# Kernel tuning notes

Measured on AMD Instinct MI355X. Metric: run time of the kernel, lower is better.

Reference implementation:

```python
import jax, jax.numpy as jnp
import numpy as np

H = 1024
B, S = 8, 2048
EPS = 1e-5


def _layernorm(x, w, b):
    m = jnp.mean(x, axis=-1, keepdims=True)
    v = jnp.mean((x - m) ** 2, axis=-1, keepdims=True)
    return (x - m) * jax.lax.rsqrt(v + EPS) * w + b


def setup_inputs() -> dict:
    key = jax.random.key(0)
    ks = jax.random.split(key, 10)
    x = jax.random.normal(ks[0], (B, S, H), dtype=jnp.float32)
    # LayerNorm params (torch default init: weight=1, bias=0)
    qn_w = jnp.ones((H,), jnp.float32)
    qn_b = jnp.zeros((H,), jnp.float32)
    kvn_w = jnp.ones((H,), jnp.float32)
    kvn_b = jnp.zeros((H,), jnp.float32)
    # q_prime/k_prime/v_prime ~ U(-0.5, 0.5)
    q_prime = jax.random.uniform(ks[1], (1, H), jnp.float32) - 0.5
    k_prime = jax.random.uniform(ks[2], (1, H), jnp.float32) - 0.5
    v_prime = jax.random.uniform(ks[3], (1, H), jnp.float32) - 0.5
    # Linear params, torch-style fan_in init
    lim = 1.0 / np.sqrt(H)
    qW = jax.random.uniform(ks[4], (H, H), jnp.float32, -lim, lim)
    qb = jax.random.uniform(ks[5], (H,), jnp.float32, -lim, lim)
    v1W = jax.random.uniform(ks[6], (H, H), jnp.float32, -lim, lim)
    v1b = jax.random.uniform(ks[7], (H,), jnp.float32, -lim, lim)
    v2W = jax.random.uniform(ks[8], (H, H), jnp.float32, -lim, lim)
    v2b = jax.random.uniform(ks[9], (H,), jnp.float32, -lim, lim)
    return {"x": x, "qn_w": qn_w, "qn_b": qn_b, "kvn_w": kvn_w, "kvn_b": kvn_b,
            "q_prime": q_prime, "k_prime": k_prime, "v_prime": v_prime,
            "qW": qW, "qb": qb, "v1W": v1W, "v1b": v1b, "v2W": v2W, "v2b": v2b}


def reference(x, qn_w, qn_b, kvn_w, kvn_b, q_prime, k_prime, v_prime,
              qW, qb, v1W, v1b, v2W, v2b):
    divisor = jnp.sqrt(jnp.float32(x.shape[-1]))
    xqn = _layernorm(x, qn_w, qn_b)            # [B,S,H]
    xkvn = _layernorm(x, kvn_w, kvn_b)         # [B,S,H]
    kr = xkvn * jax.nn.sigmoid(k_prime)        # [B,S,H]
    qr = (xqn @ qW.T + qb) * jax.nn.sigmoid(q_prime)  # [B,S,H]
    vp = jax.nn.sigmoid(v_prime)               # [1,H]
    gate = jax.nn.sigmoid(vp @ v1W.T + v1b) * jnp.tanh(vp @ v2W.T + v2b)  # [1,H]
    vr = xkvn * gate                           # [B,S,H]
    scores = jnp.einsum('bsh,bth->bst', qr, kr) / divisor  # [B,S,S]
    b, s, t = scores.shape
    # global softmax over flattened seq x seq matrix
    attn = jax.nn.softmax(scores.reshape(b, s * t), axis=-1).reshape(b, s, t)
    attended = jnp.einsum('bst,bth->bsh', attn, vr)
    return attended + xqn
```

## Files before the change

### kernel.cpp

```cpp
#include <hip/hip_runtime.h>
#include <stdint.h>


#define DEVI __device__ __forceinline__

typedef __bf16 bf16x8 __attribute__((ext_vector_type(8)));
typedef float  f32x4  __attribute__((ext_vector_type(4)));

typedef __attribute__((address_space(3))) uint32_t lds_u32_t;
typedef __attribute__((address_space(1))) uint32_t glb_u32_t;

DEVI uint16_t f2bf(float f) {
  union { float f; uint32_t u; } v; v.f = f;
  uint32_t r = (v.u + 0x7fffu + ((v.u >> 16) & 1u)) >> 16;
  return (uint16_t)r;
}
DEVI float bf2f(uint16_t b) {
  union { uint32_t u; float f; } v; v.u = ((uint32_t)b) << 16;
  return v.f;
}
DEVI float sigm(float x) { return 1.0f / (1.0f + __expf(-x)); }

DEVI void gl_lds16(const void* g, const void* lds_base) {
  __builtin_amdgcn_global_load_lds((glb_u32_t*)(uintptr_t)g,
                                   (lds_u32_t*)(uint32_t)(uintptr_t)lds_base,
                                   16, 0, 0);
}


#define SLOT (256 * 32)

DEVI void stage_half(const uint16_t* __restrict__ src, size_t ld, int kbase,
                     uint16_t* slot, int tid) {
#pragma unroll
  for (int q = 0; q < 2; q++) {
    const int idx = q * 512 + tid;
    const int r = idx >> 2;
    const int cl = (((idx & 3) ^ ((r >> 1) & 3)) * 8);
    gl_lds16(src + (size_t)r * ld + (kbase + cl),
             slot + (size_t)(q * 512 + (tid & ~63)) * 8);
  }
}

DEVI void gemm256(const uint16_t* __restrict__ A, size_t lda,
                  const uint16_t* __restrict__ B, size_t ldb,
                  int K, uint16_t* sA, uint16_t* sB, f32x4 (&acc)[8][4])
{
  const int tid = threadIdx.x, lane = tid & 63, w = tid >> 6;
  const int wr = (w >> 2) * 128, wc = (w & 3) * 64;
  const int m16 = lane & 15, quad = lane >> 4;
  const int NT = K >> 6, NH = K >> 5;

  stage_half(A, lda, 0, sA, tid);
  stage_half(B, ldb, 0, sB, tid);
  stage_half(A, lda, 32, sA + SLOT, tid);
  stage_half(B, ldb, 32, sB + SLOT, tid);
  stage_half(A, lda, 64, sA + 2 * SLOT, tid);
  stage_half(B, ldb, 64, sB + 2 * SLOT, tid);
  asm volatile("s_waitcnt vmcnt(4)" ::: "memory");
  __builtin_amdgcn_s_barrier();

  const int sw = (quad ^ ((m16 >> 1) & 3)) * 8;

  for (int t = 0; t < NT; t++) {
#pragma unroll
    for (int p = 0; p < 4; p++) {
      const int ks = p >> 1, g = p & 1;
      const uint16_t* a_s = sA + ((2 * t + ks) & 3) * SLOT;
      const uint16_t* b_s = sB + ((2 * t + ks) & 3) * SLOT;
      bf16x8 af[4], bv[4];
#pragma unroll
      for (int i = 0; i < 4; i++) {
        af[i] = *(const bf16x8*)(a_s + (wr + g * 64 + i * 16 + m16) * 32 + sw);
        bv[i] = *(const bf16x8*)(b_s + (wc + i * 16 + m16) * 32 + sw);
      }
      const int h = 2 * t + 3 + ks;
      if (h < NH) {
        if (g == 0) stage_half(A, lda, h * 32, sA + (h & 3) * SLOT, tid);
        else        stage_half(B, ldb, h * 32, sB + (h & 3) * SLOT, tid);
      }
      __builtin_amdgcn_s_barrier();
      __builtin_amdgcn_s_setprio(1);
#pragma unroll
      for (int mi = 0; mi < 4; mi++)
#pragma unroll
        for (int ni = 0; ni < 4; ni++)
          acc[g * 4 + mi][ni] = __builtin_amdgcn_mfma_f32_16x16x32_bf16(
              af[mi], bv[ni], acc[g * 4 + mi][ni], 0, 0, 0);
      __builtin_amdgcn_s_setprio(0);
      if (p == 3) {
        if (t < NT - 2) asm volatile("s_waitcnt vmcnt(4)" ::: "memory");
        else            asm volatile("s_waitcnt vmcnt(0)" ::: "memory");
      }
      __builtin_amdgcn_s_barrier();
    }
  }
}

__global__ void gate_kernel(const float* __restrict__ v_prime,
                            const float* __restrict__ v1W, const float* __restrict__ v1b,
                            const float* __restrict__ v2W, const float* __restrict__ v2b,
                            const float* __restrict__ k_prime,
                            float* __restrict__ gate2)
{
  const int tid = threadIdx.x, lane = tid & 63, w = tid >> 6;
  const int j = blockIdx.x * 4 + w;
  float d1 = 0.f, d2 = 0.f;
  for (int it = 0; it < 16; it++) {
    int i = it * 64 + lane;
    float vp = sigm(v_prime[i]);
    d1 += vp * v1W[(size_t)j * 1024 + i];
    d2 += vp * v2W[(size_t)j * 1024 + i];
  }
  for (int off = 32; off; off >>= 1) { d1 += __shfl_xor(d1, off); d2 += __shfl_xor(d2, off); }
  if (lane == 0)
    gate2[j] = sigm(d1 + v1b[j]) * tanhf(d2 + v2b[j]) / sigm(k_prime[j]);
}

__global__ void cvt_kernel(const float* __restrict__ src, uint16_t* __restrict__ dst)
{
  size_t i = ((size_t)blockIdx.x * 256 + threadIdx.x) * 4;
  float4 v = *(const float4*)(src + i);
  *(ushort4*)(dst + i) = make_ushort4(f2bf(v.x), f2bf(v.y), f2bf(v.z), f2bf(v.w));
}

__global__ __launch_bounds__(256) void ln_kernel(
    const float* __restrict__ x,
    const float* __restrict__ qn_w, const float* __restrict__ qn_b,
    const float* __restrict__ kvn_w, const float* __restrict__ kvn_b,
    const float* __restrict__ k_prime,
    uint16_t* __restrict__ xqn_bf, uint16_t* __restrict__ kr,
    float* __restrict__ krowsq)
{
  const int lane = threadIdx.x & 63, w = threadIdx.x >> 6;
  const int row = blockIdx.x * 4 + w;
  const float4* xr = (const float4*)(x + (size_t)row * 1024);
  float4 v[4];
  float s = 0.f, sq = 0.f;
#pragma unroll
  for (int i = 0; i < 4; i++) {
    v[i] = xr[i * 64 + lane];
    s  += v[i].x + v[i].y + v[i].z + v[i].w;
    sq += v[i].x * v[i].x + v[i].y * v[i].y + v[i].z * v[i].z + v[i].w * v[i].w;
  }
  for (int off = 32; off; off >>= 1) { s += __shfl_xor(s, off); sq += __shfl_xor(sq, off); }
  const float mean = s * (1.f / 1024.f);
  const float rstd = rsqrtf(sq * (1.f / 1024.f) - mean * mean + 1e-5f);

  float ksq = 0.f;
  const size_t o4 = (size_t)row * 256;
#pragma unroll
  for (int i = 0; i < 4; i++) {
    const int idx = i * 64 + lane;
    float4 qw = ((const float4*)qn_w)[idx],  qb4 = ((const float4*)qn_b)[idx];
    float4 kw = ((const float4*)kvn_w)[idx], kb4 = ((const float4*)kvn_b)[idx];
    float4 kp = ((const float4*)k_prime)[idx];
    float xn0 = (v[i].x - mean) * rstd, xn1 = (v[i].y - mean) * rstd;
    float xn2 = (v[i].z - mean) * rstd, xn3 = (v[i].w - mean) * rstd;
    float xq0 = xn0 * qw.x + qb4.x, xq1 = xn1 * qw.y + qb4.y;
    float xq2 = xn2 * qw.z + qb4.z, xq3 = xn3 * qw.w + qb4.w;
    float xk0 = xn0 * kw.x + kb4.x, xk1 = xn1 * kw.y + kb4.y;
    float xk2 = xn2 * kw.z + kb4.z, xk3 = xn3 * kw.w + kb4.w;
    float k0 = xk0 * sigm(kp.x), k1 = xk1 * sigm(kp.y);
    float k2 = xk2 * sigm(kp.z), k3 = xk3 * sigm(kp.w);
    ksq += k0 * k0 + k1 * k1 + k2 * k2 + k3 * k3;
    ((ushort4*)xqn_bf)[o4 + idx] = make_ushort4(f2bf(xq0), f2bf(xq1), f2bf(xq2), f2bf(xq3));
    ((ushort4*)kr)[o4 + idx] = make_ushort4(f2bf(k0), f2bf(k1), f2bf(k2), f2bf(k3));
  }
  for (int off = 32; off; off >>= 1) ksq += __shfl_xor(ksq, off);
  if (lane == 0) krowsq[row] = ksq;
}

__global__ __launch_bounds__(512, 2) void qr_gemm_kernel(
    const uint16_t* __restrict__ xqn_bf, const uint16_t* __restrict__ qWbf,
    const float* __restrict__ qb, const float* __restrict__ q_prime,
    uint16_t* __restrict__ qr, float* __restrict__ qnormsq)
{
  __shared__ uint16_t sA[4 * SLOT], sB[4 * SLOT];
  const int lid = blockIdx.x;
  const int c = lid >> 6, r = lid & 63;
  f32x4 acc[8][4];
#pragma unroll
  for (int i = 0; i < 8; i++)
#pragma unroll
    for (int j = 0; j < 4; j++) acc[i][j] = (f32x4)0.0f;

  gemm256(xqn_bf + (size_t)r * 256 * 1024, 1024,
          qWbf + (size_t)c * 256 * 1024, 1024, 1024, sA, sB, acc);

  const int tid = threadIdx.x, lane = tid & 63, w = tid >> 6;
  const int m16 = lane & 15, quad = lane >> 4;
  const int rbase = r * 256 + (w >> 2) * 128, cbase = c * 256 + (w & 3) * 64;
#pragma unroll
  for (int ai = 0; ai < 8; ai++) {
    const int gr0 = rbase + (ai >> 2) * 64 + (ai & 3) * 16 + quad * 4;
    float rsq[4] = {0.f, 0.f, 0.f, 0.f};
#pragma unroll
    for (int ni = 0; ni < 4; ni++) {
      const int gc = cbase + ni * 16 + m16;
      const float scale = sigm(q_prime[gc]);
      const float bias = qb[gc];
#pragma unroll
      for (int rr = 0; rr < 4; rr++) {
        float val = (acc[ai][ni][rr] + bias) * scale;
        qr[(size_t)(gr0 + rr) * 1024 + gc] = f2bf(val);
        rsq[rr] += val * val;
      }
    }
#pragma unroll
    for (int rr = 0; rr < 4; rr++) {
      float tq = rsq[rr];
      tq += __shfl_xor(tq, 1); tq += __shfl_xor(tq, 2);
      tq += __shfl_xor(tq, 4); tq += __shfl_xor(tq, 8);
      if (m16 == 0) atomicAdd(&qnormsq[gr0 + rr], tq);
    }
  }
}

__global__ void bound_kernel(const float* __restrict__ qnormsq,
                             const float* __restrict__ krowsq, float* __restrict__ MZ)
{
  const int b = blockIdx.x, tid = threadIdx.x, lane = tid & 63, w = tid >> 6;
  float mq = 0.f, mk = 0.f;
  for (int i = tid; i < 2048; i += 256) {
    mq = fmaxf(mq, qnormsq[b * 2048 + i]);
    mk = fmaxf(mk, krowsq[b * 2048 + i]);
  }
  for (int off = 32; off; off >>= 1) {
    mq = fmaxf(mq, __shfl_xor(mq, off));
    mk = fmaxf(mk, __shfl_xor(mk, off));
  }
  __shared__ float rm[4], rk[4];
  if (lane == 0) { rm[w] = mq; rk[w] = mk; }
  __syncthreads();
  if (tid == 0) {
    float qmax = fmaxf(fmaxf(rm[0], rm[1]), fmaxf(rm[2], rm[3]));
    float kmax = fmaxf(fmaxf(rk[0], rk[1]), fmaxf(rk[2], rk[3]));
    MZ[b] = sqrtf(qmax * kmax) * 0.03125f;
  }
}

__global__ void transpose_kernel(const uint16_t* __restrict__ kr,
                                 const float* __restrict__ gate2,
                                 uint16_t* __restrict__ vrt)
{
  __shared__ uint16_t t[64 * 72];
  const int b = blockIdx.z;
  const int t0 = blockIdx.x * 64, h0 = blockIdx.y * 64;
  const uint16_t* src = kr + (size_t)b * 2048 * 1024;
#pragma unroll
  for (int p = 0; p < 2; p++) {
    int flat = p * 256 + threadIdx.x;
    int r = flat >> 3, c = (flat & 7) * 8;
    *(uint4*)(&t[r * 72 + c]) = *(const uint4*)(src + (size_t)(t0 + r) * 1024 + h0 + c);
  }
  __syncthreads();
  uint16_t* dst = vrt + (size_t)b * 1024 * 2048;
#pragma unroll
  for (int p = 0; p < 2; p++) {
    int flat = p * 256 + threadIdx.x;
    int oh = flat >> 3, oc = (flat & 7) * 8;
    const float g = gate2[h0 + oh];
    union { uint16_t e[8]; uint4 v; } u;
#pragma unroll
    for (int j = 0; j < 8; j++) u.e[j] = f2bf(bf2f(t[(oc + j) * 72 + oh]) * g);
    *(uint4*)(dst + (size_t)(h0 + oh) * 2048 + t0 + oc) = u.v;
  }
}

__global__ __launch_bounds__(512, 2) void scores_kernel(
    const uint16_t* __restrict__ qr, const uint16_t* __restrict__ kr,
    const float* __restrict__ MZ,
    uint16_t* __restrict__ scores, float* __restrict__ blockZ)
{
  __shared__ uint16_t sA[4 * SLOT], sB[4 * SLOT];
  __shared__ float redz[8];
  const int lid = blockIdx.x;
  const int b = lid >> 6, c = (lid >> 3) & 7, r = lid & 7;
  f32x4 acc[8][4];
#pragma unroll
  for (int i = 0; i < 8; i++)
#pragma unroll
    for (int j = 0; j < 4; j++) acc[i][j] = (f32x4)0.0f;

  gemm256(qr + (size_t)b * 2048 * 1024 + (size_t)r * 256 * 1024, 1024,
          kr + (size_t)b * 2048 * 1024 + (size_t)c * 256 * 1024, 1024,
          1024, sA, sB, acc);

  const float Mhat = MZ[b];
  const int tid = threadIdx.x, lane = tid & 63, w = tid >> 6;
  const int m16 = lane & 15, quad = lane >> 4;
  const int rbase = r * 256 + (w >> 2) * 128, cbase = c * 256 + (w & 3) * 64;
  uint16_t* S = scores + ((size_t)b << 22);
  float zt = 0.f;
#pragma unroll
  for (int ai = 0; ai < 8; ai++) {
    const int gr0 = rbase + (ai >> 2) * 64 + (ai & 3) * 16 + quad * 4;
#pragma unroll
    for (int ni = 0; ni < 4; ni++) {
      const int gc = cbase + ni * 16 + m16;
#pragma unroll
      for (int rr = 0; rr < 4; rr++) {
        float pe = __expf(acc[ai][ni][rr] * 0.03125f - Mhat);
        zt += pe;
        S[(size_t)(gr0 + rr) * 2048 + gc] = f2bf(pe);
      }
    }
  }
  for (int off = 32; off; off >>= 1) zt += __shfl_xor(zt, off);
  if (lane == 0) redz[w] = zt;
  __syncthreads();
  if (tid == 0) {
    float sz = 0.f;
#pragma unroll
    for (int i = 0; i < 8; i++) sz += redz[i];
    blockZ[lid] = sz;
  }
}

__global__ void zreduce_kernel(const float* __restrict__ blockZ, float* __restrict__ MZ)
{
  const int b = blockIdx.x, lane = threadIdx.x;
  float z = blockZ[b * 64 + lane];
  for (int off = 32; off; off >>= 1) z += __shfl_xor(z, off);
  if (lane == 0) MZ[8 + b] = z;
}

__global__ __launch_bounds__(512, 2) void pv_gemm_kernel(
    const uint16_t* __restrict__ P, const uint16_t* __restrict__ vrt,
    const float* __restrict__ MZ, const uint16_t* __restrict__ xqn_bf,
    float* __restrict__ out)
{
  __shared__ uint16_t sA[4 * SLOT], sB[4 * SLOT];
  const int lid = blockIdx.x;
  const int b = lid >> 5, c = (lid >> 3) & 3, r = lid & 7;
  f32x4 acc[8][4];
#pragma unroll
  for (int i = 0; i < 8; i++)
#pragma unroll
    for (int j = 0; j < 4; j++) acc[i][j] = (f32x4)0.0f;

  gemm256(P + ((size_t)b << 22) + (size_t)r * 256 * 2048, 2048,
          vrt + (size_t)b * 1024 * 2048 + (size_t)c * 256 * 2048, 2048,
          2048, sA, sB, acc);

  const float invZ = 1.0f / MZ[8 + b];
  const int tid = threadIdx.x, lane = tid & 63, w = tid >> 6;
  const int m16 = lane & 15, quad = lane >> 4;
  const int rbase = r * 256 + (w >> 2) * 128, cbase = c * 256 + (w & 3) * 64;
#pragma unroll
  for (int ai = 0; ai < 8; ai++) {
    const int gr0 = rbase + (ai >> 2) * 64 + (ai & 3) * 16 + quad * 4;
#pragma unroll
    for (int ni = 0; ni < 4; ni++) {
      const int gc = cbase + ni * 16 + m16;
#pragma unroll
      for (int rr = 0; rr < 4; rr++) {
        size_t o = ((size_t)b * 2048 + gr0 + rr) * 1024 + gc;
        out[o] = acc[ai][ni][rr] * invZ + bf2f(xqn_bf[o]);
      }
    }
  }
}

extern "C" void kernel_launch(void* const* d_in, const int* in_sizes, int n_in,
                              void* d_out, int out_size, void* d_ws, size_t ws_size,
                              hipStream_t stream) {
  const float* x       = (const float*)d_in[0];
  const float* qn_w    = (const float*)d_in[1];
  const float* qn_b    = (const float*)d_in[2];
  const float* kvn_w   = (const float*)d_in[3];
  const float* kvn_b   = (const float*)d_in[4];
  const float* q_prime = (const float*)d_in[5];
  const float* k_prime = (const float*)d_in[6];
  const float* v_prime = (const float*)d_in[7];
  const float* qW      = (const float*)d_in[8];
  const float* qb      = (const float*)d_in[9];
  const float* v1W     = (const float*)d_in[10];
  const float* v1b     = (const float*)d_in[11];
  const float* v2W     = (const float*)d_in[12];
  const float* v2b     = (const float*)d_in[13];
  float* out = (float*)d_out;

  const size_t BS = 16384, H = 1024;
  char* ws = (char*)d_ws;
  size_t off = 0;
  auto alloc = [&](size_t bytes) -> char* {
    char* p = ws + off;
    off = (off + bytes + 255) & ~(size_t)255;
    return p;
  };
  float*    gate2   = (float*)alloc(H * 4);
  float*    MZ      = (float*)alloc(16 * 4);
  float*    blockZ  = (float*)alloc(2048 * 4);
  float*    qnormsq = (float*)alloc(16384 * 4);
  float*    krowsq  = (float*)alloc(16384 * 4);
  uint16_t* qWbf    = (uint16_t*)alloc(H * H * 2);
  uint16_t* xqn_bf  = (uint16_t*)alloc(BS * H * 2);
  uint16_t* kr      = (uint16_t*)alloc(BS * H * 2);
  uint16_t* scores  = (uint16_t*)alloc(BS * H * 2 * 2);
  uint16_t* vrt     = (uint16_t*)alloc(BS * H * 2);
  uint16_t* qr      = (uint16_t*)alloc(BS * H * 2);

  hipMemsetAsync(qnormsq, 0, 16384 * 4, stream);
  gate_kernel<<<256, 256, 0, stream>>>(v_prime, v1W, v1b, v2W, v2b, k_prime, gate2);
  cvt_kernel<<<1024, 256, 0, stream>>>(qW, qWbf);
  ln_kernel<<<4096, 256, 0, stream>>>(x, qn_w, qn_b, kvn_w, kvn_b, k_prime,
                                      xqn_bf, kr, krowsq);
  qr_gemm_kernel<<<256, 512, 0, stream>>>(xqn_bf, qWbf, qb, q_prime, qr, qnormsq);
  transpose_kernel<<<dim3(32, 16, 8), 256, 0, stream>>>(kr, gate2, vrt);
  bound_kernel<<<8, 256, 0, stream>>>(qnormsq, krowsq, MZ);
  scores_kernel<<<512, 512, 0, stream>>>(qr, kr, MZ, scores, blockZ);
  zreduce_kernel<<<8, 64, 0, stream>>>(blockZ, MZ);
  pv_gemm_kernel<<<256, 512, 0, stream>>>(scores, vrt, MZ, xqn_bf, out);
}
```

Baseline: 381.2 us.

## Software-pipeline LDS fragment loads one phase ahead of MFMA clusters in gemm256

Restructures the GEMM inner loop so that LDS fragment reads for the next MFMA cluster are issued before the current cluster executes, reusing B fragments across two A half-tiles instead of reloading them. Global-to-LDS staging is reordered to interleave B and A halves, and each phase uses one barrier instead of two. The aim is to hide LDS read latency behind MFMA work and cut redundant ds_reads and barriers. In exchange it raises register pressure from holding six fragment arrays, and it relies on subtle barrier and vmcnt ordering for correctness of the 4-slot ring buffer.

```diff
diff --git a/kernel.cpp b/kernel.cpp
--- a/kernel.cpp
+++ b/kernel.cpp
@@ -42,6 +42,16 @@
   }
 }
 
+#define MFMA_CLUSTER(AF, BV, GOFF)                                          \
+  __builtin_amdgcn_s_setprio(1);                                            \
+  _Pragma("unroll")                                                         \
+  for (int mi = 0; mi < 4; mi++)                                            \
+    _Pragma("unroll")                                                       \
+    for (int ni = 0; ni < 4; ni++)                                          \
+      acc[(GOFF) + mi][ni] = __builtin_amdgcn_mfma_f32_16x16x32_bf16(       \
+          AF[mi], BV[ni], acc[(GOFF) + mi][ni], 0, 0, 0);                   \
+  __builtin_amdgcn_s_setprio(0);
+
 DEVI void gemm256(const uint16_t* __restrict__ A, size_t lda,
                   const uint16_t* __restrict__ B, size_t ldb,
                   int K, uint16_t* sA, uint16_t* sB, f32x4 (&acc)[8][4])
@@ -50,50 +60,72 @@
   const int wr = (w >> 2) * 128, wc = (w & 3) * 64;
   const int m16 = lane & 15, quad = lane >> 4;
   const int NT = K >> 6, NH = K >> 5;
-
+  const int sw = (quad ^ ((m16 >> 1) & 3)) * 8;
+
+  stage_half(B, ldb, 0, sB, tid);
   stage_half(A, lda, 0, sA, tid);
-  stage_half(B, ldb, 0, sB, tid);
+  stage_half(B, ldb, 32, sB + SLOT, tid);
   stage_half(A, lda, 32, sA + SLOT, tid);
-  stage_half(B, ldb, 32, sB + SLOT, tid);
+  stage_half(B, ldb, 64, sB + 2 * SLOT, tid);
   stage_half(A, lda, 64, sA + 2 * SLOT, tid);
-  stage_half(B, ldb, 64, sB + 2 * SLOT, tid);
   asm volatile("s_waitcnt vmcnt(4)" ::: "memory");
   __builtin_amdgcn_s_barrier();
 
-  const int sw = (quad ^ ((m16 >> 1) & 3)) * 8;
+  bf16x8 bv_a[4], af_a[4], af_b[4], bv_c[4], af_c[4], af_d[4];
+#pragma unroll
+  for (int i = 0; i < 4; i++) {
+    bv_a[i] = *(const bf16x8*)(sB + (wc + i * 16 + m16) * 32 + sw);
+    af_a[i] = *(const bf16x8*)(sA + (wr + i * 16 + m16) * 32 + sw);
+  }
 
   for (int t = 0; t < NT; t++) {
-#pragma unroll
-    for (int p = 0; p < 4; p++) {
-      const int ks = p >> 1, g = p & 1;
-      const uint16_t* a_s = sA + ((2 * t + ks) & 3) * SLOT;
-      const uint16_t* b_s = sB + ((2 * t + ks) & 3) * SLOT;
-      bf16x8 af[4], bv[4];
+    const uint16_t* a0 = sA + ((2 * t) & 3) * SLOT;
+    const uint16_t* a1 = sA + ((2 * t + 1) & 3) * SLOT;
+    const uint16_t* b1 = sB + ((2 * t + 1) & 3) * SLOT;
+
+#pragma unroll
+    for (int i = 0; i < 4; i++)
+      af_b[i] = *(const bf16x8*)(a0 + (wr + 64 + i * 16 + m16) * 32 + sw);
+    if (2 * t + 3 < NH)
+      stage_half(B, ldb, (2 * t + 3) * 32, sB + ((2 * t + 3) & 3) * SLOT, tid);
+    __builtin_amdgcn_s_barrier();
+    MFMA_CLUSTER(af_a, bv_a, 0)
+
+#pragma unroll
+    for (int i = 0; i < 4; i++) {
+      bv_c[i] = *(const bf16x8*)(b1 + (wc + i * 16 + m16) * 32 + sw);
+      af_c[i] = *(const bf16x8*)(a1 + (wr + i * 16 + m16) * 32 + sw);
+    }
+    if (2 * t + 3 < NH)
+      stage_half(A, lda, (2 * t + 3) * 32, sA + ((2 * t + 3) & 3) * SLOT, tid);
+    if (t < NT - 2) asm volatile("s_waitcnt vmcnt(4)" ::: "memory");
+    else            asm volatile("s_waitcnt vmcnt(0)" ::: "memory");
+    __builtin_amdgcn_s_barrier();
+    MFMA_CLUSTER(af_b, bv_a, 4)
+
+#pragma unroll
+    for (int i = 0; i < 4; i++)
+      af_d[i] = *(const bf16x8*)(a1 + (wr + 64 + i * 16 + m16) * 32 + sw);
+    if (2 * t + 4 < NH)
+      stage_half(B, ldb, (2 * t + 4) * 32, sB + ((2 * t + 4) & 3) * SLOT, tid);
+    __builtin_amdgcn_s_barrier();
+    MFMA_CLUSTER(af_c, bv_c, 0)
+
+    if (t + 1 < NT) {
+      const uint16_t* a2 = sA + ((2 * t + 2) & 3) * SLOT;
+      const uint16_t* b2 = sB + ((2 * t + 2) & 3) * SLOT;
 #pragma unroll
       for (int i = 0; i < 4; i++) {
-        af[i] = *(const bf16x8*)(a_s + (wr + g * 64 + i * 16 + m16) * 32 + sw);
-        bv[i] = *(const bf16x8*)(b_s + (wc + i * 16 + m16) * 32 + sw);
+        bv_a[i] = *(const bf16x8*)(b2 + (wc + i * 16 + m16) * 32 + sw);
+        af_a[i] = *(const bf16x8*)(a2 + (wr + i * 16 + m16) * 32 + sw);
       }
-      const int h = 2 * t + 3 + ks;
-      if (h < NH) {
-        if (g == 0) stage_half(A, lda, h * 32, sA + (h & 3) * SLOT, tid);
-        else        stage_half(B, ldb, h * 32, sB + (h & 3) * SLOT, tid);
-      }
-      __builtin_amdgcn_s_barrier();
-      __builtin_amdgcn_s_setprio(1);
-#pragma unroll
-      for (int mi = 0; mi < 4; mi++)
-#pragma unroll
-        for (int ni = 0; ni < 4; ni++)
-          acc[g * 4 + mi][ni] = __builtin_amdgcn_mfma_f32_16x16x32_bf16(
-              af[mi], bv[ni], acc[g * 4 + mi][ni], 0, 0, 0);
-      __builtin_amdgcn_s_setprio(0);
-      if (p == 3) {
-        if (t < NT - 2) asm volatile("s_waitcnt vmcnt(4)" ::: "memory");
-        else            asm volatile("s_waitcnt vmcnt(0)" ::: "memory");
-      }
-      __builtin_amdgcn_s_barrier();
-    }
+    }
+    if (2 * t + 4 < NH)
+      stage_half(A, lda, (2 * t + 4) * 32, sA + ((2 * t + 4) & 3) * SLOT, tid);
+    if (t < NT - 2) asm volatile("s_waitcnt vmcnt(4)" ::: "memory");
+    else            asm volatile("s_waitcnt vmcnt(0)" ::: "memory");
+    __builtin_amdgcn_s_barrier();
+    MFMA_CLUSTER(af_d, bv_c, 4)
   }
 }
 
```

Measured after the change: 370.8 us. 2.7% less time.

## Shrink GEMM tiles to 128x128 with triple-buffered LDS pipeline

Applied to the files above, without the earlier changes.

Replaces the 256x256 tile, 512-thread GEMM core with a 128x128 tile, 256-thread version that uses a 3-slot LDS ring and one barrier per 32-wide K step. All three GEMM kernels (qr, scores, pv) are re-gridded with four times as many blocks, and the zreduce kernel now reduces 256 partial sums per batch. The aim is better occupancy and wave balance across the MI355X compute units, which matters because the old grids had only 256–512 blocks. The cost is less data reuse per tile, so global and L2 traffic for the A and B operands roughly doubles.

```diff
diff --git a/kernel.cpp b/kernel.cpp
--- a/kernel.cpp
+++ b/kernel.cpp
@@ -28,72 +28,66 @@
 }
 
 
-#define SLOT (256 * 32)
-
-DEVI void stage_half(const uint16_t* __restrict__ src, size_t ld, int kbase,
-                     uint16_t* slot, int tid) {
+#define SLOT128 (128 * 32)
+
+DEVI void stage_half128(const uint16_t* __restrict__ src, size_t ld, int kbase,
+                        uint16_t* slot, int tid) {
 #pragma unroll
   for (int q = 0; q < 2; q++) {
-    const int idx = q * 512 + tid;
+    const int idx = q * 256 + tid;
     const int r = idx >> 2;
     const int cl = (((idx & 3) ^ ((r >> 1) & 3)) * 8);
     gl_lds16(src + (size_t)r * ld + (kbase + cl),
-             slot + (size_t)(q * 512 + (tid & ~63)) * 8);
-  }
-}
-
-DEVI void gemm256(const uint16_t* __restrict__ A, size_t lda,
+             slot + (size_t)(q * 256 + (tid & ~63)) * 8);
+  }
+}
+
+DEVI void gemm128(const uint16_t* __restrict__ A, size_t lda,
                   const uint16_t* __restrict__ B, size_t ldb,
-                  int K, uint16_t* sA, uint16_t* sB, f32x4 (&acc)[8][4])
+                  int K, uint16_t* sA, uint16_t* sB, f32x4 (&acc)[4][4])
 {
   const int tid = threadIdx.x, lane = tid & 63, w = tid >> 6;
-  const int wr = (w >> 2) * 128, wc = (w & 3) * 64;
+  const int wr = (w >> 1) * 64, wc = (w & 1) * 64;
   const int m16 = lane & 15, quad = lane >> 4;
-  const int NT = K >> 6, NH = K >> 5;
-
-  stage_half(A, lda, 0, sA, tid);
-  stage_half(B, ldb, 0, sB, tid);
-  stage_half(A, lda, 32, sA + SLOT, tid);
-  stage_half(B, ldb, 32, sB + SLOT, tid);
-  stage_half(A, lda, 64, sA + 2 * SLOT, tid);
-  stage_half(B, ldb, 64, sB + 2 * SLOT, tid);
+  const int NH = K >> 5;
+  const int sw = (quad ^ ((m16 >> 1) & 3)) * 8;
+
+  stage_half128(B, ldb, 0, sB, tid);
+  stage_half128(A, lda, 0, sA, tid);
+  stage_half128(B, ldb, 32, sB + SLOT128, tid);
+  stage_half128(A, lda, 32, sA + SLOT128, tid);
   asm volatile("s_waitcnt vmcnt(4)" ::: "memory");
   __builtin_amdgcn_s_barrier();
 
-  const int sw = (quad ^ ((m16 >> 1) & 3)) * 8;
-
-  for (int t = 0; t < NT; t++) {
-#pragma unroll
-    for (int p = 0; p < 4; p++) {
-      const int ks = p >> 1, g = p & 1;
-      const uint16_t* a_s = sA + ((2 * t + ks) & 3) * SLOT;
-      const uint16_t* b_s = sB + ((2 * t + ks) & 3) * SLOT;
-      bf16x8 af[4], bv[4];
-#pragma unroll
-      for (int i = 0; i < 4; i++) {
-        af[i] = *(const bf16x8*)(a_s + (wr + g * 64 + i * 16 + m16) * 32 + sw);
-        bv[i] = *(const bf16x8*)(b_s + (wc + i * 16 + m16) * 32 + sw);
-      }
-      const int h = 2 * t + 3 + ks;
-      if (h < NH) {
-        if (g == 0) stage_half(A, lda, h * 32, sA + (h & 3) * SLOT, tid);
-        else        stage_half(B, ldb, h * 32, sB + (h & 3) * SLOT, tid);
-      }
-      __builtin_amdgcn_s_barrier();
-      __builtin_amdgcn_s_setprio(1);
-#pragma unroll
-      for (int mi = 0; mi < 4; mi++)
-#pragma unroll
-        for (int ni = 0; ni < 4; ni++)
-          acc[g * 4 + mi][ni] = __builtin_amdgcn_mfma_f32_16x16x32_bf16(
-              af[mi], bv[ni], acc[g * 4 + mi][ni], 0, 0, 0);
-      __builtin_amdgcn_s_setprio(0);
-      if (p == 3) {
-        if (t < NT - 2) asm volatile("s_waitcnt vmcnt(4)" ::: "memory");
-        else            asm volatile("s_waitcnt vmcnt(0)" ::: "memory");
-      }
-      __builtin_amdgcn_s_barrier();
-    }
+  int scur = 0;
+  for (int h = 0; h < NH; h++) {
+    const uint16_t* a_s = sA + scur * SLOT128;
+    const uint16_t* b_s = sB + scur * SLOT128;
+    bf16x8 af[4], bv[4];
+#pragma unroll
+    for (int i = 0; i < 4; i++) {
+      af[i] = *(const bf16x8*)(a_s + (wr + i * 16 + m16) * 32 + sw);
+      bv[i] = *(const bf16x8*)(b_s + (wc + i * 16 + m16) * 32 + sw);
+    }
+    const int h2 = h + 2;
+    if (h2 < NH) {
+      int s2 = scur + 2; if (s2 >= 3) s2 -= 3;
+      stage_half128(B, ldb, h2 * 32, sB + s2 * SLOT128, tid);
+      stage_half128(A, lda, h2 * 32, sA + s2 * SLOT128, tid);
+      asm volatile("s_waitcnt vmcnt(4)" ::: "memory");
+    } else {
+      asm volatile("s_waitcnt vmcnt(0)" ::: "memory");
+    }
+    __builtin_amdgcn_s_barrier();
+    __builtin_amdgcn_s_setprio(1);
+#pragma unroll
+    for (int mi = 0; mi < 4; mi++)
+#pragma unroll
+      for (int ni = 0; ni < 4; ni++)
+        acc[mi][ni] = __builtin_amdgcn_mfma_f32_16x16x32_bf16(
+            af[mi], bv[ni], acc[mi][ni], 0, 0, 0);
+    __builtin_amdgcn_s_setprio(0);
+    scur = (scur + 1 == 3) ? 0 : scur + 1;
   }
 }
 
@@ -171,29 +165,29 @@
   if (lane == 0) krowsq[row] = ksq;
 }
 
-__global__ __launch_bounds__(512, 2) void qr_gemm_kernel(
+__global__ __launch_bounds__(256, 3) void qr_gemm_kernel(
     const uint16_t* __restrict__ xqn_bf, const uint16_t* __restrict__ qWbf,
     const float* __restrict__ qb, const float* __restrict__ q_prime,
     uint16_t* __restrict__ qr, float* __restrict__ qnormsq)
 {
-  __shared__ uint16_t sA[4 * SLOT], sB[4 * SLOT];
+  __shared__ uint16_t sA[3 * SLOT128], sB[3 * SLOT128];
   const int lid = blockIdx.x;
-  const int c = lid >> 6, r = lid & 63;
-  f32x4 acc[8][4];
-#pragma unroll
-  for (int i = 0; i < 8; i++)
+  const int c = lid >> 7, r = lid & 127;
+  f32x4 acc[4][4];
+#pragma unroll
+  for (int i = 0; i < 4; i++)
 #pragma unroll
     for (int j = 0; j < 4; j++) acc[i][j] = (f32x4)0.0f;
 
-  gemm256(xqn_bf + (size_t)r * 256 * 1024, 1024,
-          qWbf + (size_t)c * 256 * 1024, 1024, 1024, sA, sB, acc);
+  gemm128(xqn_bf + (size_t)r * 128 * 1024, 1024,
+          qWbf + (size_t)c * 128 * 1024, 1024, 1024, sA, sB, acc);
 
   const int tid = threadIdx.x, lane = tid & 63, w = tid >> 6;
   const int m16 = lane & 15, quad = lane >> 4;
-  const int rbase = r * 256 + (w >> 2) * 128, cbase = c * 256 + (w & 3) * 64;
-#pragma unroll
-  for (int ai = 0; ai < 8; ai++) {
-    const int gr0 = rbase + (ai >> 2) * 64 + (ai & 3) * 16 + quad * 4;
+  const int rbase = r * 128 + (w >> 1) * 64, cbase = c * 128 + (w & 1) * 64;
+#pragma unroll
+  for (int mi = 0; mi < 4; mi++) {
+    const int gr0 = rbase + mi * 16 + quad * 4;
     float rsq[4] = {0.f, 0.f, 0.f, 0.f};
 #pragma unroll
     for (int ni = 0; ni < 4; ni++) {
@@ -202,7 +196,7 @@
       const float bias = qb[gc];
 #pragma unroll
       for (int rr = 0; rr < 4; rr++) {
-        float val = (acc[ai][ni][rr] + bias) * scale;
+        float val = (acc[mi][ni][rr] + bias) * scale;
         qr[(size_t)(gr0 + rr) * 1024 + gc] = f2bf(val);
         rsq[rr] += val * val;
       }
@@ -268,40 +262,40 @@
   }
 }
 
-__global__ __launch_bounds__(512, 2) void scores_kernel(
+__global__ __launch_bounds__(256, 3) void scores_kernel(
     const uint16_t* __restrict__ qr, const uint16_t* __restrict__ kr,
     const float* __restrict__ MZ,
     uint16_t* __restrict__ scores, float* __restrict__ blockZ)
 {
-  __shared__ uint16_t sA[4 * SLOT], sB[4 * SLOT];
-  __shared__ float redz[8];
+  __shared__ uint16_t sA[3 * SLOT128], sB[3 * SLOT128];
+  __shared__ float redz[4];
   const int lid = blockIdx.x;
-  const int b = lid >> 6, c = (lid >> 3) & 7, r = lid & 7;
-  f32x4 acc[8][4];
-#pragma unroll
-  for (int i = 0; i < 8; i++)
+  const int b = lid >> 8, c = (lid >> 4) & 15, r = lid & 15;
+  f32x4 acc[4][4];
+#pragma unroll
+  for (int i = 0; i < 4; i++)
 #pragma unroll
     for (int j = 0; j < 4; j++) acc[i][j] = (f32x4)0.0f;
 
-  gemm256(qr + (size_t)b * 2048 * 1024 + (size_t)r * 256 * 1024, 1024,
-          kr + (size_t)b * 2048 * 1024 + (size_t)c * 256 * 1024, 1024,
+  gemm128(qr + (size_t)b * 2048 * 1024 + (size_t)r * 128 * 1024, 1024,
+          kr + (size_t)b * 2048 * 1024 + (size_t)c * 128 * 1024, 1024,
           1024, sA, sB, acc);
 
   const float Mhat = MZ[b];
   const int tid = threadIdx.x, lane = tid & 63, w = tid >> 6;
   const int m16 = lane & 15, quad = lane >> 4;
-  const int rbase = r * 256 + (w >> 2) * 128, cbase = c * 256 + (w & 3) * 64;
+  const int rbase = r * 128 + (w >> 1) * 64, cbase = c * 128 + (w & 1) * 64;
   uint16_t* S = scores + ((size_t)b << 22);
   float zt = 0.f;
 #pragma unroll
-  for (int ai = 0; ai < 8; ai++) {
-    const int gr0 = rbase + (ai >> 2) * 64 + (ai & 3) * 16 + quad * 4;
+  for (int mi = 0; mi < 4; mi++) {
+    const int gr0 = rbase + mi * 16 + quad * 4;
 #pragma unroll
     for (int ni = 0; ni < 4; ni++) {
       const int gc = cbase + ni * 16 + m16;
 #pragma unroll
       for (int rr = 0; rr < 4; rr++) {
-        float pe = __expf(acc[ai][ni][rr] * 0.03125f - Mhat);
+        float pe = __expf(acc[mi][ni][rr] * 0.03125f - Mhat);
         zt += pe;
         S[(size_t)(gr0 + rr) * 2048 + gc] = f2bf(pe);
       }
@@ -310,54 +304,52 @@
   for (int off = 32; off; off >>= 1) zt += __shfl_xor(zt, off);
   if (lane == 0) redz[w] = zt;
   __syncthreads();
-  if (tid == 0) {
-    float sz = 0.f;
-#pragma unroll
-    for (int i = 0; i < 8; i++) sz += redz[i];
-    blockZ[lid] = sz;
-  }
+  if (tid == 0) blockZ[lid] = redz[0] + redz[1] + redz[2] + redz[3];
 }
 
 __global__ void zreduce_kernel(const float* __restrict__ blockZ, float* __restrict__ MZ)
 {
-  const int b = blockIdx.x, lane = threadIdx.x;
-  float z = blockZ[b * 64 + lane];
+  const int b = blockIdx.x, tid = threadIdx.x, lane = tid & 63, w = tid >> 6;
+  float z = blockZ[b * 256 + tid];
   for (int off = 32; off; off >>= 1) z += __shfl_xor(z, off);
-  if (lane == 0) MZ[8 + b] = z;
-}
-
-__global__ __launch_bounds__(512, 2) void pv_gemm_kernel(
+  __shared__ float rz[4];
+  if (lane == 0) rz[w] = z;
+  __syncthreads();
+  if (tid == 0) MZ[8 + b] = rz[0] + rz[1] + rz[2] + rz[3];
+}
+
+__global__ __launch_bounds__(256, 3) void pv_gemm_kernel(
     const uint16_t* __restrict__ P, const uint16_t* __restrict__ vrt,
     const float* __restrict__ MZ, const uint16_t* __restrict__ xqn_bf,
     float* __restrict__ out)
 {
-  __shared__ uint16_t sA[4 * SLOT], sB[4 * SLOT];
+  __shared__ uint16_t sA[3 * SLOT128], sB[3 * SLOT128];
   const int lid = blockIdx.x;
-  const int b = lid >> 5, c = (lid >> 3) & 3, r = lid & 7;
-  f32x4 acc[8][4];
-#pragma unroll
-  for (int i = 0; i < 8; i++)
+  const int b = lid >> 7, c = (lid >> 4) & 7, r = lid & 15;
+  f32x4 acc[4][4];
+#pragma unroll
+  for (int i = 0; i < 4; i++)
 #pragma unroll
     for (int j = 0; j < 4; j++) acc[i][j] = (f32x4)0.0f;
 
-  gemm256(P + ((size_t)b << 22) + (size_t)r * 256 * 2048, 2048,
-          vrt + (size_t)b * 1024 * 2048 + (size_t)c * 256 * 2048, 2048,
+  gemm128(P + ((size_t)b << 22) + (size_t)r * 128 * 2048, 2048,
+          vrt + (size_t)b * 1024 * 2048 + (size_t)c * 128 * 2048, 2048,
           2048, sA, sB, acc);
 
   const float invZ = 1.0f / MZ[8 + b];
   const int tid = threadIdx.x, lane = tid & 63, w = tid >> 6;
   const int m16 = lane & 15, quad = lane >> 4;
-  const int rbase = r * 256 + (w >> 2) * 128, cbase = c * 256 + (w & 3) * 64;
-#pragma unroll
-  for (int ai = 0; ai < 8; ai++) {
-    const int gr0 = rbase + (ai >> 2) * 64 + (ai & 3) * 16 + quad * 4;
+  const int rbase = r * 128 + (w >> 1) * 64, cbase = c * 128 + (w & 1) * 64;
+#pragma unroll
+  for (int mi = 0; mi < 4; mi++) {
+    const int gr0 = rbase + mi * 16 + quad * 4;
 #pragma unroll
     for (int ni = 0; ni < 4; ni++) {
       const int gc = cbase + ni * 16 + m16;
 #pragma unroll
       for (int rr = 0; rr < 4; rr++) {
         size_t o = ((size_t)b * 2048 + gr0 + rr) * 1024 + gc;
-        out[o] = acc[ai][ni][rr] * invZ + bf2f(xqn_bf[o]);
+        out[o] = acc[mi][ni][rr] * invZ + bf2f(xqn_bf[o]);
       }
     }
   }
@@ -407,10 +399,10 @@
   cvt_kernel<<<1024, 256, 0, stream>>>(qW, qWbf);
   ln_kernel<<<4096, 256, 0, stream>>>(x, qn_w, qn_b, kvn_w, kvn_b, k_prime,
                                       xqn_bf, kr, krowsq);
-  qr_gemm_kernel<<<256, 512, 0, stream>>>(xqn_bf, qWbf, qb, q_prime, qr, qnormsq);
+  qr_gemm_kernel<<<1024, 256, 0, stream>>>(xqn_bf, qWbf, qb, q_prime, qr, qnormsq);
   transpose_kernel<<<dim3(32, 16, 8), 256, 0, stream>>>(kr, gate2, vrt);
   bound_kernel<<<8, 256, 0, stream>>>(qnormsq, krowsq, MZ);
-  scores_kernel<<<512, 512, 0, stream>>>(qr, kr, MZ, scores, blockZ);
-  zreduce_kernel<<<8, 64, 0, stream>>>(blockZ, MZ);
-  pv_gemm_kernel<<<256, 512, 0, stream>>>(scores, vrt, MZ, xqn_bf, out);
-}
+  scores_kernel<<<2048, 256, 0, stream>>>(qr, kr, MZ, scores, blockZ);
+  zreduce_kernel<<<8, 256, 0, stream>>>(blockZ, MZ);
+  pv_gemm_kernel<<<1024, 256, 0, stream>>>(scores, vrt, MZ, xqn_bf, out);
+}
```

After: 396.5 us. 1.04x slower.
